# Optimization experiments

Hardware: AMD Instinct MI355X
Metric: run time of the kernel (lower is better)

## Reference

```python
import jax, jax.numpy as jnp
import numpy as np

B, H, W, DIM = 8, 32, 32, 768
HEADS = 12
HD = DIM // HEADS  # 64


def setup_inputs() -> dict:
    key = jax.random.key(0)
    ks = jax.random.split(key, 7)
    s = 0.02  # init scale to keep logits in a sane range
    return {
        "x": jax.random.normal(ks[0], (B, H, W, DIM), jnp.float32),
        "qkv_w": jax.random.normal(ks[1], (3 * DIM, DIM), jnp.float32) * s,
        "qkv_b": jax.random.normal(ks[2], (3 * DIM,), jnp.float32) * s,
        "proj_w": jax.random.normal(ks[3], (DIM, DIM), jnp.float32) * s,
        "proj_b": jax.random.normal(ks[4], (DIM,), jnp.float32) * s,
        "rel_pos_h": jax.random.normal(ks[5], (2 * H - 1, HD), jnp.float32) * s,
        "rel_pos_w": jax.random.normal(ks[6], (2 * W - 1, HD), jnp.float32) * s,
    }


def reference(x, qkv_w, qkv_b, proj_w, proj_b, rel_pos_h, rel_pos_w):
    b, h, w, dim = x.shape
    n = h * w
    hd = dim // HEADS
    scale = hd ** -0.5

    xf = x.reshape(b, n, dim)
    qkv = xf @ qkv_w.T + qkv_b                       # (B, N, 3*dim)
    qkv = qkv.reshape(b, n, 3, HEADS, hd)
    qkv = jnp.transpose(qkv, (2, 0, 3, 1, 4)).reshape(3, b * HEADS, n, hd)
    q, k, v = qkv[0], qkv[1], qkv[2]                 # each (B*heads, N, hd)

    # decomposed rel-pos bias (q_size == k_size -> pure index lookup)
    coords_h = jnp.arange(h)[:, None] - jnp.arange(h)[None, :] + (h - 1)
    coords_w = jnp.arange(w)[:, None] - jnp.arange(w)[None, :] + (w - 1)
    Rh = rel_pos_h[coords_h]                         # (H, H, hd)
    Rw = rel_pos_w[coords_w]                         # (W, W, hd)
    r_q = q.reshape(b * HEADS, h, w, hd)
    rel_h = jnp.einsum('bhwc,hkc->bhwk', r_q, Rh)    # (B*heads, H, W, H)
    rel_w = jnp.einsum('bhwc,wkc->bhwk', r_q, Rw)    # (B*heads, H, W, W)
    bias = (rel_h[:, :, :, :, None] + rel_w[:, :, :, None, :]).reshape(b * HEADS, n, n)

    attn = (q * scale) @ jnp.swapaxes(k, -2, -1) + bias
    attn = jax.nn.softmax(attn, axis=-1)
    out = attn @ v                                   # (B*heads, N, hd)

    out = out.reshape(b, HEADS, n, hd)
    out = jnp.transpose(out, (0, 2, 1, 3)).reshape(b, n, dim)
    out = out @ proj_w.T + proj_b
    return out.reshape(b, h, w, dim)
```

## Files before the change

kernel.cpp:

```cpp
#include <hip/hip_runtime.h>
#include <hip/hip_bf16.h>

typedef unsigned short u16;
typedef __attribute__((ext_vector_type(8))) short bf16x8;
typedef __attribute__((ext_vector_type(4))) short s16x4;
typedef __attribute__((ext_vector_type(4))) float f32x4;

#define QSCALE 0.18033688011116012f
#define RPSCALE 8.0f
#define EXP2(x) __builtin_amdgcn_exp2f(x)

__device__ __forceinline__ float bf2f(u16 u) {
  union { unsigned int i; float f; } v; v.i = ((unsigned int)u) << 16; return v.f;
}
__device__ __forceinline__ u16 f2bf(float f) {
  union { float f; unsigned int i; } v; v.f = f;
  unsigned int r = v.i + 0x7fffu + ((v.i >> 16) & 1u);
  return (u16)(r >> 16);
}
__device__ __forceinline__ unsigned int pk2bf(float a, float b) {
  union { __hip_bfloat162 h; unsigned int u; } cv;
  cv.h = __float22bfloat162_rn(float2{a, b});
  return cv.u;
}
__device__ __forceinline__ f32x4 MFMA(bf16x8 a, bf16x8 b, f32x4 c) {
  return __builtin_amdgcn_mfma_f32_16x16x32_bf16(a, b, c, 0, 0, 0);
}
__device__ __forceinline__ void cvt8(const float* p, uint4* dst) {
  float4 f0 = *(const float4*)(p);
  float4 f1 = *(const float4*)(p + 4);
  u16* t = (u16*)dst;
  t[0] = f2bf(f0.x); t[1] = f2bf(f0.y); t[2] = f2bf(f0.z); t[3] = f2bf(f0.w);
  t[4] = f2bf(f1.x); t[5] = f2bf(f1.y); t[6] = f2bf(f1.z); t[7] = f2bf(f1.w);
}
__device__ __forceinline__ void cvt8s(const float* p, uint4* dst, float s) {
  float4 f0 = *(const float4*)(p);
  float4 f1 = *(const float4*)(p + 4);
  u16* t = (u16*)dst;
  t[0] = f2bf(f0.x * s); t[1] = f2bf(f0.y * s); t[2] = f2bf(f0.z * s); t[3] = f2bf(f0.w * s);
  t[4] = f2bf(f1.x * s); t[5] = f2bf(f1.y * s); t[6] = f2bf(f1.z * s); t[7] = f2bf(f1.w * s);
}
__device__ __forceinline__ void gld16(const u16* g, u16* l) {
  __builtin_amdgcn_global_load_lds(
      (const __attribute__((address_space(1))) unsigned int*)g,
      (__attribute__((address_space(3))) unsigned int*)l, 16, 0, 0);
}

#define N8_X  786432
#define N8_QW 221184
#define N8_PW 73728
__global__ __launch_bounds__(256) void cast_kernel(
    const float* __restrict__ x, const float* __restrict__ qw, const float* __restrict__ pw,
    u16* __restrict__ xb, u16* __restrict__ qwb, u16* __restrict__ pwb)
{
  const int i = blockIdx.x * 256 + threadIdx.x;
  const float* s; u16* d; int off;
  if (i < N8_X)            { s = x;  d = xb;  off = i; }
  else if (i < N8_X+N8_QW) { s = qw; d = qwb; off = i - N8_X; }
  else                     { s = pw; d = pwb; off = i - (N8_X + N8_QW); }
  uint4 pk; cvt8(s + (size_t)off * 8, &pk);
  *(uint4*)(d + (size_t)off * 8) = pk;
}

__global__ __launch_bounds__(512) void gemm_qkv_8p(
    const u16* __restrict__ A, const u16* __restrict__ Bw, const float* __restrict__ bias,
    u16* __restrict__ Cq, u16* __restrict__ C1, u16* __restrict__ C2)
{
  extern __shared__ u16 lds[];
  u16* const sA = lds;
  u16* const sB = lds + 32768;
  const int tid = threadIdx.x;
  const int w = tid >> 6, lane = tid & 63;
  const int l16 = lane & 15, quad = lane >> 4;
  const int bi = blockIdx.x;
  const int u = bi >> 3;
  const int tm = ((u & 3) << 3) | (bi & 7);
  const int tn = u >> 2;
  const int m0 = tm << 8, n0 = tn << 8;

  const int srow = (w << 3) + (lane >> 3);
  const int sslot = (((lane & 7) ^ (lane >> 3)) << 3);
  const int wch = w << 9;
  const int s7 = l16 & 7;
  const int sl0 = ((quad ^ s7) << 3);
  const int sl1 = (((4 + quad) ^ s7) << 3);

#define STAGE_A8(cb, kt, h) do { \
    const u16* g_ = A + (size_t)(m0 + (h)*128 + srow)*768 + (kt)*64 + sslot; \
    gld16(g_,              sA + (cb)*16384 + (h)*8192 + wch); \
    gld16(g_ + 64*768,     sA + (cb)*16384 + (h)*8192 + 4096 + wch); \
  } while (0)
#define STAGE_B8(cb, kt, h) do { \
    const u16* g_ = Bw + (size_t)(n0 + (h)*128 + srow)*768 + (kt)*64 + sslot; \
    gld16(g_,              sB + (cb)*16384 + (h)*8192 + wch); \
    gld16(g_ + 64*768,     sB + (cb)*16384 + (h)*8192 + 4096 + wch); \
  } while (0)

  f32x4 acc[16][2];
  #pragma unroll
  for (int i = 0; i < 16; ++i)
    #pragma unroll
    for (int j = 0; j < 2; ++j) {
      acc[i][j][0] = 0.f; acc[i][j][1] = 0.f; acc[i][j][2] = 0.f; acc[i][j][3] = 0.f;
    }

  STAGE_B8(0, 0, 0);
  STAGE_B8(0, 0, 1);
  STAGE_A8(0, 0, 0);
  STAGE_A8(0, 0, 1);
  asm volatile("s_waitcnt vmcnt(2)" ::: "memory");
  __builtin_amdgcn_s_barrier();

#define PHASE8(mq, STAGE_STMT, TAIL_STMT) { \
    bf16x8 af[4][2]; \
    _Pragma("unroll") \
    for (int i = 0; i < 4; ++i) { \
      const u16* ap_ = aRd + ((mq)*64 + i*16)*64; \
      af[i][0] = *(const bf16x8*)(ap_ + sl0); \
      af[i][1] = *(const bf16x8*)(ap_ + sl1); \
    } \
    STAGE_STMT; \
    __builtin_amdgcn_s_barrier(); \
    asm volatile("s_waitcnt lgkmcnt(0)" ::: "memory"); \
    __builtin_amdgcn_sched_barrier(0); \
    __builtin_amdgcn_s_setprio(1); \
    _Pragma("unroll") \
    for (int i = 0; i < 4; ++i) { \
      acc[(mq)*4+i][0] = MFMA(af[i][0], bq[0][0], acc[(mq)*4+i][0]); \
      acc[(mq)*4+i][0] = MFMA(af[i][1], bq[0][1], acc[(mq)*4+i][0]); \
      acc[(mq)*4+i][1] = MFMA(af[i][0], bq[1][0], acc[(mq)*4+i][1]); \
      acc[(mq)*4+i][1] = MFMA(af[i][1], bq[1][1], acc[(mq)*4+i][1]); \
    } \
    __builtin_amdgcn_s_setprio(0); \
    TAIL_STMT; \
    __builtin_amdgcn_s_barrier(); \
  }

  int cur = 0;
  #pragma unroll 1
  for (int t = 0; t < 12; ++t) {
    const int t1 = (t < 11) ? t + 1 : 11;
    const int nb = cur ^ 1;
    const u16* aRd = sA + cur * 16384 + l16 * 64;
    bf16x8 bq[2][2];
    {
      const u16* bp = sB + cur * 16384 + (w * 32 + l16) * 64;
      bq[0][0] = *(const bf16x8*)(bp + sl0);
      bq[0][1] = *(const bf16x8*)(bp + sl1);
      bq[1][0] = *(const bf16x8*)(bp + 1024 + sl0);
      bq[1][1] = *(const bf16x8*)(bp + 1024 + sl1);
    }
    PHASE8(0, STAGE_B8(nb, t1, 0), {});
    PHASE8(1, STAGE_B8(nb, t1, 1), asm volatile("s_waitcnt vmcnt(4)" ::: "memory"));
    PHASE8(2, STAGE_A8(nb, t1, 0), {});
    PHASE8(3, STAGE_A8(nb, t1, 1), asm volatile("s_waitcnt vmcnt(2)" ::: "memory"));
    cur = nb;
  }
#undef PHASE8
#undef STAGE_A8
#undef STAGE_B8

  asm volatile("s_waitcnt vmcnt(0)" ::: "memory");

  const int which = tn / 3;
  #pragma unroll
  for (int j = 0; j < 2; ++j) {
    const int n = n0 + w * 32 + j * 16 + l16;
    const float bv = bias[n];
    const int rem = n - which * 768;
    const int head = rem >> 6, c = rem & 63;
    #pragma unroll
    for (int i = 0; i < 16; ++i) {
      const int m = m0 + i * 16 + quad * 4;
      const int b = m >> 10, npos = m & 1023;
      const size_t bh = (size_t)(b * 12 + head);
      if (which == 0) {
        #pragma unroll
        for (int r = 0; r < 4; ++r)
          Cq[(bh << 16) + ((size_t)(npos + r) << 6) + c] =
              f2bf((acc[i][j][r] + bv) * QSCALE);
      } else if (which == 1) {
        const size_t base = ((bh * 16 + (size_t)(npos >> 6)) << 12)
                          + (size_t)((((npos >> 4) & 3) * 2 + (c >> 5)) << 9)
                          + (size_t)((((npos & 15) + 16 * ((c >> 3) & 3)) << 3) + (c & 7));
        #pragma unroll
        for (int r = 0; r < 4; ++r)
          C1[base + r * 8] = f2bf(acc[i][j][r] + bv);
      } else {
        const size_t base = ((bh * 16 + (size_t)(npos >> 6)) << 12)
                          + (size_t)(((((npos >> 5) & 1) * 4 + (c >> 4))) << 9)
                          + (size_t)((((c & 15) + 16 * ((npos >> 3) & 3)) << 3) + (npos & 7));
        s16x4 pk;
        #pragma unroll
        for (int r = 0; r < 4; ++r) pk[r] = (short)f2bf(acc[i][j][r] + bv);
        *(s16x4*)(C2 + base) = pk;
      }
    }
  }
}

template<int MODE, int NXB>
__global__ __launch_bounds__(256) void gemm_bt(
    const u16* __restrict__ A, const u16* __restrict__ Bw, const float* __restrict__ bias,
    void* __restrict__ C0v, u16* __restrict__ C1, u16* __restrict__ C2,
    int M, int N, int K)
{
  __shared__ u16 sA[128 * 32];
  __shared__ u16 sB[128 * 32];
  const int tid = threadIdx.x;
  const int lane = tid & 63, wv = tid >> 6;
  const int wr = wv >> 1, wc = wv & 1;
  const int l16 = lane & 15, quad = lane >> 4;
  const int bi = blockIdx.x;
  const int t = bi >> 3;
  const int nx = t % NXB;
  const int my = ((t / NXB) << 3) | (bi & 7);
  const int m0 = my << 7, n0 = nx << 7;

  const int srow = tid >> 2, scol = (tid & 3) << 3;
  const u16* gA0 = A  + (size_t)(m0 + srow) * K + scol;
  const u16* gB0 = Bw + (size_t)(n0 + srow) * K + scol;
  const u16* gA1 = gA0 + (size_t)64 * K;
  const u16* gB1 = gB0 + (size_t)64 * K;
  u16* const lwA0 = sA + wv * 512;
  u16* const lwA1 = sA + 2048 + wv * 512;
  u16* const lwB0 = sB + wv * 512;
  u16* const lwB1 = sB + 2048 + wv * 512;

  f32x4 acc[4][4];
  #pragma unroll
  for (int i = 0; i < 4; ++i)
    #pragma unroll
    for (int j = 0; j < 4; ++j) {
      acc[i][j][0] = 0.f; acc[i][j][1] = 0.f; acc[i][j][2] = 0.f; acc[i][j][3] = 0.f;
    }

  for (int k0 = 0; k0 < K; k0 += 32) {
    __syncthreads();
    gld16(gA0 + k0, lwA0);
    gld16(gA1 + k0, lwA1);
    gld16(gB0 + k0, lwB0);
    gld16(gB1 + k0, lwB1);
    __syncthreads();
    bf16x8 af[4], bfr[4];
    #pragma unroll
    for (int i = 0; i < 4; ++i)
      af[i] = *(const bf16x8*)(sA + (wr * 64 + i * 16 + l16) * 32 + quad * 8);
    #pragma unroll
    for (int j = 0; j < 4; ++j)
      bfr[j] = *(const bf16x8*)(sB + (wc * 64 + j * 16 + l16) * 32 + quad * 8);
    #pragma unroll
    for (int i = 0; i < 4; ++i)
      #pragma unroll
      for (int j = 0; j < 4; ++j)
        acc[i][j] = MFMA(af[i], bfr[j], acc[i][j]);
  }

  #pragma unroll
  for (int j = 0; j < 4; ++j) {
    const int n = n0 + wc * 64 + j * 16 + l16;
    const float bv = bias[n];
    if (MODE == 0) {
      float* C0 = (float*)C0v;
      #pragma unroll
      for (int i = 0; i < 4; ++i) {
        const int m = m0 + wr * 64 + i * 16 + quad * 4;
        #pragma unroll
        for (int r = 0; r < 4; ++r)
          C0[(size_t)(m + r) * N + n] = acc[i][j][r] + bv;
      }
    } else {
      u16* C0 = (u16*)C0v;
      const int which = n / 768;
      const int rem = n - which * 768;
      const int head = rem >> 6, c = rem & 63;
      #pragma unroll
      for (int i = 0; i < 4; ++i) {
        const int m = m0 + wr * 64 + i * 16 + quad * 4;
        const int b = m >> 10, npos = m & 1023;
        const size_t bh = (size_t)(b * 12 + head);
        if (which == 0) {
          #pragma unroll
          for (int r = 0; r < 4; ++r)
            C0[(bh << 16) + ((size_t)(npos + r) << 6) + c] =
                f2bf((acc[i][j][r] + bv) * QSCALE);
        } else if (which == 1) {
          const size_t base = ((bh * 16 + (size_t)(npos >> 6)) << 12)
                            + (size_t)((((npos >> 4) & 3) * 2 + (c >> 5)) << 9)
                            + (size_t)((((npos & 15) + 16 * ((c >> 3) & 3)) << 3) + (c & 7));
          #pragma unroll
          for (int r = 0; r < 4; ++r)
            C1[base + r * 8] = f2bf(acc[i][j][r] + bv);
        } else {
          const size_t base = ((bh * 16 + (size_t)(npos >> 6)) << 12)
                            + (size_t)(((((npos >> 5) & 1) * 4 + (c >> 4))) << 9)
                            + (size_t)((((c & 15) + 16 * ((npos >> 3) & 3)) << 3) + (npos & 7));
          s16x4 pk;
          #pragma unroll
          for (int r = 0; r < 4; ++r) pk[r] = (short)f2bf(acc[i][j][r] + bv);
          *(s16x4*)(C2 + base) = pk;
        }
      }
    }
  }
}

__global__ __launch_bounds__(256) void attn_kernel(
    const u16* __restrict__ Q, const u16* __restrict__ Kf, const u16* __restrict__ Vf,
    const float* __restrict__ rph, const float* __restrict__ rpw,
    u16* __restrict__ Oa)
{
  __shared__ __align__(16) u16 uni[9216];
  __shared__ u16 sSh[4 * 32 * 36];

  u16* const uRPH = uni;
  u16* const uRPW = uni + 4536;

  const int tid = threadIdx.x;
  const int wave = tid >> 6, lane = tid & 63;
  const int l16 = lane & 15, quad = lane >> 4;
  const int bi = blockIdx.x;
  const int t = bi >> 3;
  const int qb = t & 7;
  const int bh = ((t >> 3) << 3) | (bi & 7);
  const int qrow0 = (qb << 7) + (wave << 5);
  const int qh = qrow0 >> 5;

  u16* const pw = uni + wave * 2304;
  u16* const sShw = sSh + wave * 1152;

  bf16x8 qf[2][2];
  #pragma unroll
  for (int qt = 0; qt < 2; ++qt) {
    const u16* qp = Q + (((size_t)bh << 10) + qrow0 + qt * 16 + l16) * 64 + quad * 8;
    qf[qt][0] = *(const bf16x8*)(qp);
    qf[qt][1] = *(const bf16x8*)(qp + 32);
  }

  for (int j = tid; j < 64 * 8; j += 256) {
    const int row = j >> 3, ck = (j & 7) << 3;
    uint4 vw;
    if (row < 63) cvt8s(rpw + (size_t)row * 64 + ck, &vw, RPSCALE);
    else { vw.x = 0u; vw.y = 0u; vw.z = 0u; vw.w = 0u; }
    *(uint4*)(uRPW + row * 72 + ck) = vw;
    if (row < 63) {
      uint4 vh;
      cvt8s(rph + (size_t)row * 64 + ck, &vh, RPSCALE);
      *(uint4*)(uRPH + row * 72 + ck) = vh;
    }
  }
  __syncthreads();

  #pragma unroll
  for (int qt = 0; qt < 2; ++qt)
    #pragma unroll
    for (int tk = 0; tk < 2; ++tk) {
      const int kh = tk * 16 + l16;
      const u16* bp = uRPH + (qh + 31 - kh) * 72 + quad * 8;
      bf16x8 b0 = *(const bf16x8*)(bp);
      bf16x8 b1 = *(const bf16x8*)(bp + 32);
      f32x4 c; c[0] = 0.f; c[1] = 0.f; c[2] = 0.f; c[3] = 0.f;
      c = MFMA(qf[qt][0], b0, c);
      c = MFMA(qf[qt][1], b1, c);
      #pragma unroll
      for (int r = 0; r < 4; ++r)
        sShw[(qt * 16 + quad * 4 + r) * 36 + tk * 16 + l16] = f2bf(c[r]);
    }

  f32x4 swc[2][4];
  #pragma unroll
  for (int qt = 0; qt < 2; ++qt)
    #pragma unroll
    for (int tj = 0; tj < 4; ++tj) {
      const u16* bp = uRPW + (tj * 16 + l16) * 72 + quad * 8;
      bf16x8 b0 = *(const bf16x8*)(bp);
      bf16x8 b1 = *(const bf16x8*)(bp + 32);
      f32x4 c; c[0] = 0.f; c[1] = 0.f; c[2] = 0.f; c[3] = 0.f;
      c = MFMA(qf[qt][0], b0, c);
      c = MFMA(qf[qt][1], b1, c);
      swc[qt][tj] = c;
    }
  __syncthreads();

  #pragma unroll
  for (int qt = 0; qt < 2; ++qt)
    #pragma unroll
    for (int tj = 0; tj < 4; ++tj)
      #pragma unroll
      for (int r = 0; r < 4; ++r)
        pw[(qt * 16 + quad * 4 + r) * 72 + tj * 16 + l16] = f2bf(swc[qt][tj][r]);

  float rw[2][2][4];
  #pragma unroll
  for (int qt = 0; qt < 2; ++qt)
    #pragma unroll
    for (int hi = 0; hi < 2; ++hi)
      #pragma unroll
      for (int r = 0; r < 4; ++r) {
        const int kw = hi * 16 + quad * 4 + r;
        rw[qt][hi][r] = bf2f(pw[(qt * 16 + l16) * 72 + (qt * 16 + l16 - kw + 31)]);
      }

  f32x4 oacc[2][4];
  #pragma unroll
  for (int qt = 0; qt < 2; ++qt)
    #pragma unroll
    for (int nd = 0; nd < 4; ++nd) {
      oacc[qt][nd][0] = 0.f; oacc[qt][nd][1] = 0.f;
      oacc[qt][nd][2] = 0.f; oacc[qt][nd][3] = 0.f;
    }
  float lsum[2] = {0.f, 0.f};

  const u16* const Kfb = Kf + (((size_t)bh) << 16) + lane * 8;
  const u16* const Vfb = Vf + (((size_t)bh) << 16) + lane * 8;

  for (int kt = 0; kt < 16; ++kt) {
    const u16* Kp = Kfb + ((size_t)kt << 12);
    const u16* Vp = Vfb + ((size_t)kt << 12);
    bf16x8 kfr[8];
    #pragma unroll
    for (int m = 0; m < 8; ++m)
      kfr[m] = *(const bf16x8*)(Kp + (m << 9));
    #pragma unroll
    for (int m = 0; m < 8; ++m)
      asm volatile("" :: "v"(kfr[m]));

    float rh[2][2];
    #pragma unroll
    for (int qt = 0; qt < 2; ++qt) {
      const unsigned int w2 =
          *(const unsigned int*)(sShw + (qt * 16 + l16) * 36 + (kt << 1));
      rh[qt][0] = bf2f((u16)(w2 & 0xffffu));
      rh[qt][1] = bf2f((u16)(w2 >> 16));
    }

    #pragma unroll
    for (int qt = 0; qt < 2; ++qt) {
      f32x4 sacc[4];
      #pragma unroll
      for (int mk = 0; mk < 4; ++mk) {
        f32x4 t4; t4[0] = 0.f; t4[1] = 0.f; t4[2] = 0.f; t4[3] = 0.f;
        t4 = MFMA(kfr[mk * 2 + 0], qf[qt][0], t4);
        t4 = MFMA(kfr[mk * 2 + 1], qf[qt][1], t4);
        sacc[mk] = t4;
      }
      #pragma unroll
      for (int mk = 0; mk < 4; ++mk) {
        const float rhv = rh[qt][mk >> 1];
        const float* rwp = rw[qt][mk & 1];
        float e0 = EXP2(sacc[mk][0] + rhv + rwp[0]);
        float e1 = EXP2(sacc[mk][1] + rhv + rwp[1]);
        float e2 = EXP2(sacc[mk][2] + rhv + rwp[2]);
        float e3 = EXP2(sacc[mk][3] + rhv + rwp[3]);
        lsum[qt] += (e0 + e1) + (e2 + e3);
        uint2 pk2; pk2.x = pk2bf(e0, e1); pk2.y = pk2bf(e2, e3);
        *(uint2*)(pw + (qt * 16 + l16) * 72 + mk * 16 + quad * 4) = pk2;
      }
    }

    #pragma unroll
    for (int ks = 0; ks < 2; ++ks) {
      bf16x8 bv[4];
      #pragma unroll
      for (int nd = 0; nd < 4; ++nd)
        bv[nd] = *(const bf16x8*)(Vp + ((ks * 4 + nd) << 9));
      #pragma unroll
      for (int qt = 0; qt < 2; ++qt) {
        bf16x8 ap = *(const bf16x8*)(pw + (qt * 16 + l16) * 72 + ks * 32 + quad * 8);
        #pragma unroll
        for (int nd = 0; nd < 4; ++nd)
          oacc[qt][nd] = MFMA(bv[nd], ap, oacc[qt][nd]);
      }
    }
  }

  const int b = bh / 12, head = bh - b * 12;
  #pragma unroll
  for (int qt = 0; qt < 2; ++qt) {
    float ls = lsum[qt];
    ls += __shfl_xor(ls, 16);
    ls += __shfl_xor(ls, 32);
    const float linv = 1.0f / ls;
    const size_t base =
        ((size_t)(b << 10) + qrow0 + qt * 16 + l16) * 768 + head * 64 + quad * 4;
    #pragma unroll
    for (int nd = 0; nd < 4; ++nd) {
      s16x4 pk;
      #pragma unroll
      for (int r = 0; r < 4; ++r) pk[r] = (short)f2bf(oacc[qt][nd][r] * linv);
      *(s16x4*)(Oa + base + nd * 16) = pk;
    }
  }
}

extern "C" void kernel_launch(void* const* d_in, const int* in_sizes, int n_in,
                              void* d_out, int out_size, void* d_ws, size_t ws_size,
                              hipStream_t stream) {
  (void)in_sizes; (void)n_in; (void)out_size; (void)ws_size;
  const float* x      = (const float*)d_in[0];
  const float* qkv_w  = (const float*)d_in[1];
  const float* qkv_b  = (const float*)d_in[2];
  const float* proj_w = (const float*)d_in[3];
  const float* proj_b = (const float*)d_in[4];
  const float* rph    = (const float*)d_in[5];
  const float* rpw    = (const float*)d_in[6];
  float* out = (float*)d_out;

  char* ws = (char*)d_ws;
  const size_t SZ = (size_t)96 * 1024 * 64;
  u16* Qw  = (u16*)ws;
  u16* Kfw = Qw + SZ;
  u16* Vfw = Kfw + SZ;
  u16* Xb  = Vfw + SZ;
  u16* Oa  = Xb;
  u16* QWb = Xb + SZ;
  u16* PWb = QWb + (size_t)2304 * 768;

  static bool attr_set = false;
  if (!attr_set) {
    (void)hipFuncSetAttribute((const void*)gemm_qkv_8p,
                              hipFuncAttributeMaxDynamicSharedMemorySize, 131072);
    attr_set = true;
  }

  cast_kernel<<<4224, 256, 0, stream>>>(x, qkv_w, proj_w, Xb, QWb, PWb);
  gemm_qkv_8p<<<288, 512, 131072, stream>>>(Xb, QWb, qkv_b, Qw, Kfw, Vfw);
  attn_kernel<<<768, 256, 0, stream>>>(Qw, Kfw, Vfw, rph, rpw, Oa);
  gemm_bt<0, 6><<<384, 256, 0, stream>>>(Oa, PWb, proj_b, out, nullptr, nullptr, 8192, 768, 768);
}
```

Measured before the change: 213.4 us.

## Retile QKV GEMM to 128x192 tiles with 256-thread blocks

Changes the QKV projection GEMM from 256x256 tiles with 512-thread blocks (288 blocks, 128KB LDS) to 128x192 tiles with 256-thread blocks (768 blocks, 80KB LDS). Each wave now computes 128x48 instead of 256x32. The staging, the wait counts and the epilogue head mapping are reworked to match. The aim is better load balance across the 256 CUs, since 288 blocks leave a ragged second wave, at the cost of lower arithmetic intensity per tile.

```diff
diff --git a/kernel.cpp b/kernel.cpp
--- a/kernel.cpp
+++ b/kernel.cpp
@@ -62,62 +62,56 @@
   *(uint4*)(d + (size_t)off * 8) = pk;
 }
 
-__global__ __launch_bounds__(512) void gemm_qkv_8p(
+__global__ __launch_bounds__(256) void gemm_qkv_8p(
     const u16* __restrict__ A, const u16* __restrict__ Bw, const float* __restrict__ bias,
     u16* __restrict__ Cq, u16* __restrict__ C1, u16* __restrict__ C2)
 {
   extern __shared__ u16 lds[];
-  u16* const sA = lds;
-  u16* const sB = lds + 32768;
+  u16* const sAl = lds;
+  u16* const sBl = lds + 16384;
   const int tid = threadIdx.x;
   const int w = tid >> 6, lane = tid & 63;
   const int l16 = lane & 15, quad = lane >> 4;
   const int bi = blockIdx.x;
   const int u = bi >> 3;
-  const int tm = ((u & 3) << 3) | (bi & 7);
-  const int tn = u >> 2;
-  const int m0 = tm << 8, n0 = tn << 8;
-
-  const int srow = (w << 3) + (lane >> 3);
-  const int sslot = (((lane & 7) ^ (lane >> 3)) << 3);
+  const int tn = u >> 3;
+  const int tm = ((u & 7) << 3) | (bi & 7);
+  const int m0 = tm << 7;
+  const int n0 = tn * 192;
+
+  const int rstag = tid >> 3;
+  const int gslot = (((tid & 7) ^ ((tid >> 3) & 7)) << 3);
   const int wch = w << 9;
   const int s7 = l16 & 7;
   const int sl0 = ((quad ^ s7) << 3);
   const int sl1 = (((4 + quad) ^ s7) << 3);
 
-#define STAGE_A8(cb, kt, h) do { \
-    const u16* g_ = A + (size_t)(m0 + (h)*128 + srow)*768 + (kt)*64 + sslot; \
-    gld16(g_,              sA + (cb)*16384 + (h)*8192 + wch); \
-    gld16(g_ + 64*768,     sA + (cb)*16384 + (h)*8192 + 4096 + wch); \
-  } while (0)
-#define STAGE_B8(cb, kt, h) do { \
-    const u16* g_ = Bw + (size_t)(n0 + (h)*128 + srow)*768 + (kt)*64 + sslot; \
-    gld16(g_,              sB + (cb)*16384 + (h)*8192 + wch); \
-    gld16(g_ + 64*768,     sB + (cb)*16384 + (h)*8192 + 4096 + wch); \
-  } while (0)
-
-  f32x4 acc[16][2];
-  #pragma unroll
-  for (int i = 0; i < 16; ++i)
-    #pragma unroll
-    for (int j = 0; j < 2; ++j) {
+#define STAGE_B(cb, kt, s) gld16(Bw + (size_t)(n0 + (s)*32 + rstag)*768 + (kt)*64 + gslot, \
+                                 sBl + (cb)*12288 + (s)*2048 + wch)
+#define STAGE_A(cb, kt, s) gld16(A + (size_t)(m0 + (s)*32 + rstag)*768 + (kt)*64 + gslot, \
+                                 sAl + (cb)*8192 + (s)*2048 + wch)
+
+  f32x4 acc[8][3];
+  #pragma unroll
+  for (int i = 0; i < 8; ++i)
+    #pragma unroll
+    for (int j = 0; j < 3; ++j) {
       acc[i][j][0] = 0.f; acc[i][j][1] = 0.f; acc[i][j][2] = 0.f; acc[i][j][3] = 0.f;
     }
 
-  STAGE_B8(0, 0, 0);
-  STAGE_B8(0, 0, 1);
-  STAGE_A8(0, 0, 0);
-  STAGE_A8(0, 0, 1);
+  STAGE_B(0, 0, 0); STAGE_B(0, 0, 1); STAGE_B(0, 0, 2);
+  STAGE_B(0, 0, 3); STAGE_B(0, 0, 4); STAGE_B(0, 0, 5);
+  STAGE_A(0, 0, 0); STAGE_A(0, 0, 1); STAGE_A(0, 0, 2); STAGE_A(0, 0, 3);
   asm volatile("s_waitcnt vmcnt(2)" ::: "memory");
   __builtin_amdgcn_s_barrier();
 
-#define PHASE8(mq, STAGE_STMT, TAIL_STMT) { \
-    bf16x8 af[4][2]; \
+#define PHASEQ(p, STAGE_STMT, TAIL_STMT) { \
+    bf16x8 af[2][2]; \
     _Pragma("unroll") \
-    for (int i = 0; i < 4; ++i) { \
-      const u16* ap_ = aRd + ((mq)*64 + i*16)*64; \
-      af[i][0] = *(const bf16x8*)(ap_ + sl0); \
-      af[i][1] = *(const bf16x8*)(ap_ + sl1); \
+    for (int ii = 0; ii < 2; ++ii) { \
+      const u16* ap_ = aRd + (((p)*2 + ii) * 16) * 64; \
+      af[ii][0] = *(const bf16x8*)(ap_ + sl0); \
+      af[ii][1] = *(const bf16x8*)(ap_ + sl1); \
     } \
     STAGE_STMT; \
     __builtin_amdgcn_s_barrier(); \
@@ -125,12 +119,12 @@
     __builtin_amdgcn_sched_barrier(0); \
     __builtin_amdgcn_s_setprio(1); \
     _Pragma("unroll") \
-    for (int i = 0; i < 4; ++i) { \
-      acc[(mq)*4+i][0] = MFMA(af[i][0], bq[0][0], acc[(mq)*4+i][0]); \
-      acc[(mq)*4+i][0] = MFMA(af[i][1], bq[0][1], acc[(mq)*4+i][0]); \
-      acc[(mq)*4+i][1] = MFMA(af[i][0], bq[1][0], acc[(mq)*4+i][1]); \
-      acc[(mq)*4+i][1] = MFMA(af[i][1], bq[1][1], acc[(mq)*4+i][1]); \
-    } \
+    for (int ii = 0; ii < 2; ++ii) \
+      _Pragma("unroll") \
+      for (int j = 0; j < 3; ++j) { \
+        acc[(p)*2+ii][j] = MFMA(af[ii][0], bq[j][0], acc[(p)*2+ii][j]); \
+        acc[(p)*2+ii][j] = MFMA(af[ii][1], bq[j][1], acc[(p)*2+ii][j]); \
+      } \
     __builtin_amdgcn_s_setprio(0); \
     TAIL_STMT; \
     __builtin_amdgcn_s_barrier(); \
@@ -141,36 +135,39 @@
   for (int t = 0; t < 12; ++t) {
     const int t1 = (t < 11) ? t + 1 : 11;
     const int nb = cur ^ 1;
-    const u16* aRd = sA + cur * 16384 + l16 * 64;
-    bf16x8 bq[2][2];
+    const u16* aRd = sAl + cur * 8192 + l16 * 64;
+    bf16x8 bq[3][2];
     {
-      const u16* bp = sB + cur * 16384 + (w * 32 + l16) * 64;
-      bq[0][0] = *(const bf16x8*)(bp + sl0);
-      bq[0][1] = *(const bf16x8*)(bp + sl1);
-      bq[1][0] = *(const bf16x8*)(bp + 1024 + sl0);
-      bq[1][1] = *(const bf16x8*)(bp + 1024 + sl1);
-    }
-    PHASE8(0, STAGE_B8(nb, t1, 0), {});
-    PHASE8(1, STAGE_B8(nb, t1, 1), asm volatile("s_waitcnt vmcnt(4)" ::: "memory"));
-    PHASE8(2, STAGE_A8(nb, t1, 0), {});
-    PHASE8(3, STAGE_A8(nb, t1, 1), asm volatile("s_waitcnt vmcnt(2)" ::: "memory"));
+      const u16* bp = sBl + cur * 12288 + (w * 48 + l16) * 64;
+      #pragma unroll
+      for (int j = 0; j < 3; ++j) {
+        bq[j][0] = *(const bf16x8*)(bp + j * 1024 + sl0);
+        bq[j][1] = *(const bf16x8*)(bp + j * 1024 + sl1);
+      }
+    }
+    PHASEQ(0, { STAGE_B(nb, t1, 0); STAGE_B(nb, t1, 1); STAGE_B(nb, t1, 2); }, {});
+    PHASEQ(1, { STAGE_B(nb, t1, 3); STAGE_B(nb, t1, 4); STAGE_B(nb, t1, 5); },
+              asm volatile("s_waitcnt vmcnt(6)" ::: "memory"));
+    PHASEQ(2, { STAGE_A(nb, t1, 0); STAGE_A(nb, t1, 1); }, {});
+    PHASEQ(3, { STAGE_A(nb, t1, 2); STAGE_A(nb, t1, 3); },
+              asm volatile("s_waitcnt vmcnt(2)" ::: "memory"));
     cur = nb;
   }
-#undef PHASE8
-#undef STAGE_A8
-#undef STAGE_B8
+#undef PHASEQ
+#undef STAGE_A
+#undef STAGE_B
 
   asm volatile("s_waitcnt vmcnt(0)" ::: "memory");
 
-  const int which = tn / 3;
-  #pragma unroll
-  for (int j = 0; j < 2; ++j) {
-    const int n = n0 + w * 32 + j * 16 + l16;
+  const int which = tn >> 2;
+  #pragma unroll
+  for (int j = 0; j < 3; ++j) {
+    const int n = n0 + w * 48 + j * 16 + l16;
     const float bv = bias[n];
     const int rem = n - which * 768;
     const int head = rem >> 6, c = rem & 63;
     #pragma unroll
-    for (int i = 0; i < 16; ++i) {
+    for (int i = 0; i < 8; ++i) {
       const int m = m0 + i * 16 + quad * 4;
       const int b = m >> 10, npos = m & 1023;
       const size_t bh = (size_t)(b * 12 + head);
@@ -519,12 +516,12 @@
   static bool attr_set = false;
   if (!attr_set) {
     (void)hipFuncSetAttribute((const void*)gemm_qkv_8p,
-                              hipFuncAttributeMaxDynamicSharedMemorySize, 131072);
+                              hipFuncAttributeMaxDynamicSharedMemorySize, 81920);
     attr_set = true;
   }
 
   cast_kernel<<<4224, 256, 0, stream>>>(x, qkv_w, proj_w, Xb, QWb, PWb);
-  gemm_qkv_8p<<<288, 512, 131072, stream>>>(Xb, QWb, qkv_b, Qw, Kfw, Vfw);
+  gemm_qkv_8p<<<768, 256, 81920, stream>>>(Xb, QWb, qkv_b, Qw, Kfw, Vfw);
   attn_kernel<<<768, 256, 0, stream>>>(Qw, Kfw, Vfw, rph, rpw, Oa);
   gemm_bt<0, 6><<<384, 256, 0, stream>>>(Oa, PWb, proj_b, out, nullptr, nullptr, 8192, 768, 768);
 }
```

New measurement: 214.3 us. About the same (+0.4%).
